# Kernel optimization log

Measured on AMD Instinct MI355X. Metric: run time of the kernel, lower is better.

Reference implementation:

```python
import jax, jax.numpy as jnp
import numpy as np

N, S, R, CM = 1, 128, 256, 256
C, CZ = 32, 128


def setup_inputs() -> dict:
    key = jax.random.key(0)
    k1, k2, k3, k4 = jax.random.split(key, 4)
    return {
        "msa_repr": jax.random.normal(k1, (N, S, R, CM), dtype=jnp.float32),
        "left_proj": jax.random.normal(k2, (CM, C), dtype=jnp.float32) * 0.05,
        "right_proj": jax.random.normal(k3, (CM, C), dtype=jnp.float32) * 0.05,
        "out_proj": jax.random.normal(k4, (C * C, CZ), dtype=jnp.float32) * 0.05,
    }


def reference(msa_repr, left_proj, right_proj, out_proj):
    # msa_repr: [N, S, R, CM]
    # Project to left/right activations and move R before S
    # (equivalent to torch matmul + transpose(-2, -3)).
    a = jnp.einsum("nsrm,mc->nrsc", msa_repr, left_proj)   # [N, R, S, C]
    b = jnp.einsum("nsrm,mc->nrsc", msa_repr, right_proj)  # [N, R, S, C]
    # Outer product contracted over the MSA dim S:
    # outer[n, r, t, c, e] = sum_s a[n, r, s, c] * b[n, t, s, e]
    outer = jnp.einsum("nrsc,ntse->nrtce", a, b)            # [N, R, R, C, C]
    n, r, t = outer.shape[:3]
    outer = outer.reshape(n, r, t, C * C)                   # [N, R, R, C*C]
    # Output projection to pair channels cz
    return outer @ out_proj                                 # [N, R, R, CZ]
```

## Files before the change

kernel.cpp:

```cpp
#include <hip/hip_runtime.h>

typedef __bf16 bf16x8 __attribute__((ext_vector_type(8)));
typedef __bf16 bf16x4 __attribute__((ext_vector_type(4)));
typedef float f32x16 __attribute__((ext_vector_type(16)));
typedef float f32x4 __attribute__((ext_vector_type(4)));

constexpr int S = 128, R = 256, CM = 256, C = 32, CZ = 128;

#define MFMA __builtin_amdgcn_mfma_f32_32x32x16_bf16

__device__ __forceinline__ bf16x4 cvt4(float a, float b, float c, float d) {
    bf16x4 r;
    r[0] = (__bf16)a; r[1] = (__bf16)b; r[2] = (__bf16)c; r[3] = (__bf16)d;
    return r;
}

__global__ __launch_bounds__(256) void k_wlr(const float* __restrict__ Lp,
                                             const float* __restrict__ Rp,
                                             __bf16* __restrict__ WLRT) {
    int c = blockIdx.x;
    int m = threadIdx.x;
    const float* src = (c < 32) ? Lp : Rp;
    WLRT[(size_t)c * 256 + m] = (__bf16)src[(size_t)m * 32 + (c & 31)];
}

__global__ __launch_bounds__(256) void k_projw(const float* __restrict__ msa,
                                               const __bf16* __restrict__ WLRT,
                                               const float* __restrict__ W,
                                               __bf16* __restrict__ aTf,
                                               __bf16* __restrict__ bTf,
                                               __bf16* __restrict__ WTf) {
    const int b = blockIdx.x;
    if (b >= 1024) {
        int g = (b - 1024) * 256 + threadIdx.x;
        int cz = g & 127;
        int k = g >> 7;
        int e = k >> 5, c = k & 31;
        float v = W[(size_t)(c * 32 + e) * 128 + cz];
        WTf[((size_t)(k >> 3) * 128 + cz) * 8 + (k & 7)] = (__bf16)v;
        return;
    }

    __shared__ __align__(16) __bf16 As[32 * 256];
    __shared__ __align__(16) char Pp[2 * 4096];
    const int r = b >> 2;
    const int sq = b & 3;
    const int t = threadIdx.x;

#pragma unroll
    for (int it = 0; it < 8; ++it) {
        int idx = it * 256 + t;
        int row = idx >> 6;
        int cg = idx & 63;
        float4 v = *(const float4*)&msa[((size_t)(sq * 32 + row) * R + r) * CM + cg * 4];
        bf16x4 h = cvt4(v.x, v.y, v.z, v.w);
        int P = (cg >> 1) ^ (row & 15);
        *(bf16x4*)((char*)As + row * 512 + P * 16 + (cg & 1) * 8) = h;
    }
    __syncthreads();

    const int w = t >> 6;
    const int l = t & 63;
    const int l31 = t & 31;
    const int kh = (t >> 5) & 1;
    const int sd = w & 1;
    const int ksh = w >> 1;

    f32x16 acc;
#pragma unroll
    for (int q = 0; q < 16; ++q) acc[q] = 0.f;

    const bf16x8* wb = (const bf16x8*)&WLRT[(size_t)(sd * 32 + l31) * 256 + 8 * kh];
    const char* arow = (const char*)As + l31 * 512;

    __builtin_amdgcn_s_setprio(1);
#pragma unroll
    for (int j = 0; j < 8; ++j) {
        int ks = ksh * 8 + j;
        int P = (2 * ks + kh) ^ (l31 & 15);
        bf16x8 af = *(const bf16x8*)(arow + P * 16);
        acc = MFMA(af, wb[2 * ks], acc, 0, 0, 0);
    }
    __builtin_amdgcn_s_setprio(0);

    char* pbase = Pp + (size_t)sd * 4096;
    if (ksh == 1) {
#pragma unroll
        for (int pc = 0; pc < 4; ++pc) {
            f32x4 v;
            v[0] = acc[4 * pc + 0]; v[1] = acc[4 * pc + 1];
            v[2] = acc[4 * pc + 2]; v[3] = acc[4 * pc + 3];
            *(f32x4*)(pbase + ((pc * 64) + l) * 16) = v;
        }
    }
    __syncthreads();
    if (ksh == 0) {
#pragma unroll
        for (int pc = 0; pc < 4; ++pc) {
            f32x4 v = *(const f32x4*)(pbase + ((pc * 64) + l) * 16);
            acc[4 * pc + 0] += v[0]; acc[4 * pc + 1] += v[1];
            acc[4 * pc + 2] += v[2]; acc[4 * pc + 3] += v[3];
        }
        __bf16* dst = sd ? bTf : aTf;
#pragma unroll
        for (int q = 0; q < 4; ++q) {
            size_t base = (size_t)r * 4096 + (size_t)(2 * sq + (q >> 1)) * 512 +
                          (size_t)(q & 1) * 256 + (size_t)l31 * 8 + 4 * kh;
            *(bf16x4*)&dst[base] = cvt4(acc[4 * q + 0], acc[4 * q + 1],
                                        acc[4 * q + 2], acc[4 * q + 3]);
        }
    }
}

__global__ __launch_bounds__(512, 2) void k_main(const __bf16* __restrict__ aTf,
                                                 const __bf16* __restrict__ bTf,
                                                 const __bf16* __restrict__ WTf,
                                                 float* __restrict__ out) {
    __shared__ __align__(16) __bf16 Gs[64 * 1024];

    const int t = threadIdx.x;
    const int w = t >> 6;
    const int l = t & 63;
    const int lane = l & 31;
    const int kh = l >> 5;
    const int r0 = blockIdx.x * 8;
    const int t0 = blockIdx.y * 8;

    const int rg = w & 3;
    const int tg = w >> 2;

    f32x16 acc[2][4];
#pragma unroll
    for (int i = 0; i < 2; ++i)
#pragma unroll
        for (int j = 0; j < 4; ++j)
#pragma unroll
            for (int q = 0; q < 16; ++q) acc[i][j][q] = 0.f;

    const bf16x8* ap0 = (const bf16x8*)aTf + ((size_t)(r0 + 2 * rg + 0) * 512 + kh * 32 + lane);
    const bf16x8* ap1 = (const bf16x8*)aTf + ((size_t)(r0 + 2 * rg + 1) * 512 + kh * 32 + lane);
    const bf16x8* bp0 = (const bf16x8*)bTf + ((size_t)(t0 + 4 * tg + 0) * 512 + kh * 32 + lane);
    const bf16x8* bp1 = (const bf16x8*)bTf + ((size_t)(t0 + 4 * tg + 1) * 512 + kh * 32 + lane);
    const bf16x8* bp2 = (const bf16x8*)bTf + ((size_t)(t0 + 4 * tg + 2) * 512 + kh * 32 + lane);
    const bf16x8* bp3 = (const bf16x8*)bTf + ((size_t)(t0 + 4 * tg + 3) * 512 + kh * 32 + lane);

    bf16x8 Ap[3][2], Bp[3][4];
#pragma unroll
    for (int s = 0; s < 3; ++s) {
        Ap[s][0] = ap0[s * 64]; Ap[s][1] = ap1[s * 64];
        Bp[s][0] = bp0[s * 64]; Bp[s][1] = bp1[s * 64];
        Bp[s][2] = bp2[s * 64]; Bp[s][3] = bp3[s * 64];
    }
#pragma unroll
    for (int ks = 0; ks < 8; ++ks) {
        const int s = ks % 3;
        __builtin_amdgcn_s_setprio(1);
        acc[0][0] = MFMA(Ap[s][0], Bp[s][0], acc[0][0], 0, 0, 0);
        acc[0][1] = MFMA(Ap[s][0], Bp[s][1], acc[0][1], 0, 0, 0);
        acc[0][2] = MFMA(Ap[s][0], Bp[s][2], acc[0][2], 0, 0, 0);
        acc[0][3] = MFMA(Ap[s][0], Bp[s][3], acc[0][3], 0, 0, 0);
        acc[1][0] = MFMA(Ap[s][1], Bp[s][0], acc[1][0], 0, 0, 0);
        acc[1][1] = MFMA(Ap[s][1], Bp[s][1], acc[1][1], 0, 0, 0);
        acc[1][2] = MFMA(Ap[s][1], Bp[s][2], acc[1][2], 0, 0, 0);
        acc[1][3] = MFMA(Ap[s][1], Bp[s][3], acc[1][3], 0, 0, 0);
        __builtin_amdgcn_s_setprio(0);
        if (ks + 3 < 8) {
            const int kn = ks + 3;
            Ap[s][0] = ap0[kn * 64]; Ap[s][1] = ap1[kn * 64];
            Bp[s][0] = bp0[kn * 64]; Bp[s][1] = bp1[kn * 64];
            Bp[s][2] = bp2[kn * 64]; Bp[s][3] = bp3[kn * 64];
        }
    }

    const int kq = w >> 1;
    const int ng = w & 1;
    const int czl0 = ng * 64 + lane;
    const int czl1 = czl0 + 32;
    const char* wb0c = (const char*)WTf + ((size_t)kh * 128 + czl0) * 16;
    const char* wb1c = (const char*)WTf + ((size_t)kh * 128 + czl1) * 16;

    bf16x8 Wp[16][2];
#pragma unroll
    for (int i = 0; i < 2; ++i) {
#pragma unroll
        for (int j = 0; j < 4; ++j) {
            int p = (2 * rg + i) * 8 + 4 * tg + j;
            unsigned prow = (unsigned)p * 2048;
#pragma unroll
            for (int q = 0; q < 4; ++q) {
                int Lc = lane * 4 + q;
                int P = Lc ^ (p & 15) ^ (lane & 7);
                *(bf16x4*)((char*)Gs + prow + (unsigned)P * 16 + kh * 8) =
                    cvt4(acc[i][j][4 * q + 0], acc[i][j][4 * q + 1],
                         acc[i][j][4 * q + 2], acc[i][j][4 * q + 3]);
            }
            {
                const int u = i * 4 + j;
                const char* a0 = wb0c + (size_t)(kq * 16 + 2 * u) * 4096;
                const char* a1 = wb1c + (size_t)(kq * 16 + 2 * u) * 4096;
                const char* a2 = wb0c + (size_t)(kq * 16 + 2 * u + 1) * 4096;
                const char* a3 = wb1c + (size_t)(kq * 16 + 2 * u + 1) * 4096;
                asm volatile("global_load_dwordx4 %0, %1, off" : "=v"(Wp[2 * u][0]) : "v"(a0));
                asm volatile("global_load_dwordx4 %0, %1, off" : "=v"(Wp[2 * u][1]) : "v"(a1));
                asm volatile("global_load_dwordx4 %0, %1, off" : "=v"(Wp[2 * u + 1][0]) : "v"(a2));
                asm volatile("global_load_dwordx4 %0, %1, off" : "=v"(Wp[2 * u + 1][1]) : "v"(a3));
            }
        }
    }

    asm volatile("s_waitcnt lgkmcnt(0)" ::: "memory");
    __builtin_amdgcn_s_barrier();
    __builtin_amdgcn_sched_barrier(0);

    const unsigned prow0 = (unsigned)lane * 2048;
    const unsigned prow1 = (unsigned)(lane + 32) * 2048;
    const int p15 = lane & 15;

    f32x16 o00, o01, o10, o11;
#pragma unroll
    for (int q = 0; q < 16; ++q) { o00[q] = 0.f; o01[q] = 0.f; o10[q] = 0.f; o11[q] = 0.f; }

    bf16x8 Gp[4][2];
#define LDG(sl, kk) do { \
    int Lr = (kk) * 2 + kh; \
    int P = Lr ^ p15 ^ ((Lr >> 2) & 7); \
    Gp[sl][0] = *(const bf16x8*)((const char*)Gs + prow0 + (unsigned)P * 16); \
    Gp[sl][1] = *(const bf16x8*)((const char*)Gs + prow1 + (unsigned)P * 16); } while (0)

    LDG(0, kq * 16 + 0);
    LDG(1, kq * 16 + 1);
    LDG(2, kq * 16 + 2);
    LDG(3, kq * 16 + 3);

#define STEPB(j, cnt) do { \
    asm volatile("s_waitcnt vmcnt(" #cnt ")"); \
    __builtin_amdgcn_sched_barrier(0); \
    __builtin_amdgcn_s_setprio(1); \
    o00 = MFMA(Gp[(j) & 3][0], Wp[j][0], o00, 0, 0, 0); \
    o01 = MFMA(Gp[(j) & 3][0], Wp[j][1], o01, 0, 0, 0); \
    o10 = MFMA(Gp[(j) & 3][1], Wp[j][0], o10, 0, 0, 0); \
    o11 = MFMA(Gp[(j) & 3][1], Wp[j][1], o11, 0, 0, 0); \
    __builtin_amdgcn_s_setprio(0); \
    if ((j) + 4 < 16) LDG((j) & 3, kq * 16 + (j) + 4); \
} while (0)

    STEPB(0, 30);  STEPB(1, 28);  STEPB(2, 26);  STEPB(3, 24);
    STEPB(4, 22);  STEPB(5, 20);  STEPB(6, 18);  STEPB(7, 16);
    STEPB(8, 14);  STEPB(9, 12);  STEPB(10, 10); STEPB(11, 8);
    STEPB(12, 6);  STEPB(13, 4);  STEPB(14, 2);  STEPB(15, 0);

    __syncthreads();

    {
        char* pr = (char*)Gs + (size_t)w * 16384;
        const f32x16* os[4] = {&o00, &o01, &o10, &o11};
#pragma unroll
        for (int s2 = 0; s2 < 4; ++s2) {
#pragma unroll
            for (int pc = 0; pc < 4; ++pc) {
                f32x4 v;
                v[0] = (*os[s2])[4 * pc + 0]; v[1] = (*os[s2])[4 * pc + 1];
                v[2] = (*os[s2])[4 * pc + 2]; v[3] = (*os[s2])[4 * pc + 3];
                *(f32x4*)(pr + ((s2 * 4 + pc) * 64 + l) * 16) = v;
            }
        }
    }
    __syncthreads();

    {
        const int ngx = w >> 2;
        const int mix = (w >> 1) & 1;
        const int nix = w & 1;
        const int s2 = mix * 2 + nix;
        f32x16 sm;
#pragma unroll
        for (int q = 0; q < 16; ++q) sm[q] = 0.f;
#pragma unroll
        for (int kq2 = 0; kq2 < 4; ++kq2) {
            const char* pr = (const char*)Gs + (size_t)(kq2 * 2 + ngx) * 16384;
#pragma unroll
            for (int pc = 0; pc < 4; ++pc) {
                f32x4 v = *(const f32x4*)(pr + ((s2 * 4 + pc) * 64 + l) * 16);
                sm[4 * pc + 0] += v[0]; sm[4 * pc + 1] += v[1];
                sm[4 * pc + 2] += v[2]; sm[4 * pc + 3] += v[3];
            }
        }
        const int czl = ngx * 64 + nix * 32 + (l & 31);
        const int khx = l >> 5;
#pragma unroll
        for (int reg = 0; reg < 16; ++reg) {
            int pl = mix * 32 + (reg & 3) + 8 * (reg >> 2) + 4 * khx;
            int prr = pl >> 3, ptt = pl & 7;
            out[((size_t)(r0 + prr) * 256 + (t0 + ptt)) * 128 + czl] = sm[reg];
        }
    }
}

extern "C" void kernel_launch(void* const* d_in, const int* in_sizes, int n_in,
                              void* d_out, int out_size, void* d_ws, size_t ws_size,
                              hipStream_t stream) {
    const float* msa = (const float*)d_in[0];
    const float* left = (const float*)d_in[1];
    const float* right = (const float*)d_in[2];
    const float* W = (const float*)d_in[3];

    __bf16* aTf = (__bf16*)d_ws;
    __bf16* bTf = aTf + (size_t)R * 4096;
    __bf16* WTf = bTf + (size_t)R * 4096;
    __bf16* WLRT = WTf + (size_t)128 * 1024;
    float* outp = (float*)d_out;

    k_wlr<<<64, 256, 0, stream>>>(left, right, WLRT);
    k_projw<<<1536, 256, 0, stream>>>(msa, WLRT, W, aTf, bTf, WTf);
    k_main<<<dim3(32, 32), 512, 0, stream>>>(aTf, bTf, WTf, outp);
}
```

Baseline: 59.32 us.

## Repartition output-projection K split across waves to shrink cross-wave reduction

The second GEMM (outer-product tile times out_proj) now splits the K dimension two ways instead of four, with each wave owning one 32-wide cz slice. W fragments are streamed through an 8-deep rolling register buffer instead of being preloaded as 32 registers. This removes one of the shared-memory partial-sum round trips and replaces a four-way reduction with a two-way one, so less LDS traffic and fewer registers are needed. In exchange each wave runs a longer serial MFMA chain and depends more on W load latency being hidden.

Measured after the change: 58.12 us (median of 2 runs). 1.02x faster.

```diff
diff --git a/kernel.cpp b/kernel.cpp
--- a/kernel.cpp
+++ b/kernel.cpp
@@ -172,14 +172,12 @@
         }
     }
 
-    const int kq = w >> 1;
-    const int ng = w & 1;
-    const int czl0 = ng * 64 + lane;
-    const int czl1 = czl0 + 32;
-    const char* wb0c = (const char*)WTf + ((size_t)kh * 128 + czl0) * 16;
-    const char* wb1c = (const char*)WTf + ((size_t)kh * 128 + czl1) * 16;
-
-    bf16x8 Wp[16][2];
+    const int kq = w >> 2;
+    const int ng = w & 3;
+    const int czl = ng * 32 + lane;
+    const char* wbc = (const char*)WTf + ((size_t)kh * 128 + czl) * 16;
+
+    bf16x8 Wp[8];
 #pragma unroll
     for (int i = 0; i < 2; ++i) {
 #pragma unroll
@@ -196,14 +194,8 @@
             }
             {
                 const int u = i * 4 + j;
-                const char* a0 = wb0c + (size_t)(kq * 16 + 2 * u) * 4096;
-                const char* a1 = wb1c + (size_t)(kq * 16 + 2 * u) * 4096;
-                const char* a2 = wb0c + (size_t)(kq * 16 + 2 * u + 1) * 4096;
-                const char* a3 = wb1c + (size_t)(kq * 16 + 2 * u + 1) * 4096;
-                asm volatile("global_load_dwordx4 %0, %1, off" : "=v"(Wp[2 * u][0]) : "v"(a0));
-                asm volatile("global_load_dwordx4 %0, %1, off" : "=v"(Wp[2 * u][1]) : "v"(a1));
-                asm volatile("global_load_dwordx4 %0, %1, off" : "=v"(Wp[2 * u + 1][0]) : "v"(a2));
-                asm volatile("global_load_dwordx4 %0, %1, off" : "=v"(Wp[2 * u + 1][1]) : "v"(a3));
+                asm volatile("global_load_dwordx4 %0, %1, off"
+                             : "=v"(Wp[u]) : "v"(wbc + (size_t)(kq * 32 + u) * 4096));
             }
         }
     }
@@ -216,82 +208,81 @@
     const unsigned prow1 = (unsigned)(lane + 32) * 2048;
     const int p15 = lane & 15;
 
-    f32x16 o00, o01, o10, o11;
-#pragma unroll
-    for (int q = 0; q < 16; ++q) { o00[q] = 0.f; o01[q] = 0.f; o10[q] = 0.f; o11[q] = 0.f; }
+    f32x16 o0, o1;
+#pragma unroll
+    for (int q = 0; q < 16; ++q) { o0[q] = 0.f; o1[q] = 0.f; }
 
     bf16x8 Gp[4][2];
-#define LDG(sl, kk) do { \
-    int Lr = (kk) * 2 + kh; \
+#define LDG(sl, j) do { \
+    int Lr = (kq * 32 + (j)) * 2 + kh; \
     int P = Lr ^ p15 ^ ((Lr >> 2) & 7); \
     Gp[sl][0] = *(const bf16x8*)((const char*)Gs + prow0 + (unsigned)P * 16); \
     Gp[sl][1] = *(const bf16x8*)((const char*)Gs + prow1 + (unsigned)P * 16); } while (0)
 
-    LDG(0, kq * 16 + 0);
-    LDG(1, kq * 16 + 1);
-    LDG(2, kq * 16 + 2);
-    LDG(3, kq * 16 + 3);
+    LDG(0, 0); LDG(1, 1); LDG(2, 2); LDG(3, 3);
 
 #define STEPB(j, cnt) do { \
     asm volatile("s_waitcnt vmcnt(" #cnt ")"); \
     __builtin_amdgcn_sched_barrier(0); \
     __builtin_amdgcn_s_setprio(1); \
-    o00 = MFMA(Gp[(j) & 3][0], Wp[j][0], o00, 0, 0, 0); \
-    o01 = MFMA(Gp[(j) & 3][0], Wp[j][1], o01, 0, 0, 0); \
-    o10 = MFMA(Gp[(j) & 3][1], Wp[j][0], o10, 0, 0, 0); \
-    o11 = MFMA(Gp[(j) & 3][1], Wp[j][1], o11, 0, 0, 0); \
+    o0 = MFMA(Gp[(j) & 3][0], Wp[(j) & 7], o0, 0, 0, 0); \
+    o1 = MFMA(Gp[(j) & 3][1], Wp[(j) & 7], o1, 0, 0, 0); \
     __builtin_amdgcn_s_setprio(0); \
-    if ((j) + 4 < 16) LDG((j) & 3, kq * 16 + (j) + 4); \
+    if ((j) + 8 < 32) { \
+        asm volatile("global_load_dwordx4 %0, %1, off" \
+                     : "=v"(Wp[(j) & 7]) \
+                     : "v"(wbc + (size_t)(kq * 32 + (j) + 8) * 4096)); \
+    } \
+    if ((j) + 4 < 32) LDG((j) & 3, (j) + 4); \
 } while (0)
 
-    STEPB(0, 30);  STEPB(1, 28);  STEPB(2, 26);  STEPB(3, 24);
-    STEPB(4, 22);  STEPB(5, 20);  STEPB(6, 18);  STEPB(7, 16);
-    STEPB(8, 14);  STEPB(9, 12);  STEPB(10, 10); STEPB(11, 8);
-    STEPB(12, 6);  STEPB(13, 4);  STEPB(14, 2);  STEPB(15, 0);
-
-    __syncthreads();
-
-    {
-        char* pr = (char*)Gs + (size_t)w * 16384;
-        const f32x16* os[4] = {&o00, &o01, &o10, &o11};
-#pragma unroll
-        for (int s2 = 0; s2 < 4; ++s2) {
-#pragma unroll
-            for (int pc = 0; pc < 4; ++pc) {
-                f32x4 v;
-                v[0] = (*os[s2])[4 * pc + 0]; v[1] = (*os[s2])[4 * pc + 1];
-                v[2] = (*os[s2])[4 * pc + 2]; v[3] = (*os[s2])[4 * pc + 3];
-                *(f32x4*)(pr + ((s2 * 4 + pc) * 64 + l) * 16) = v;
-            }
-        }
-    }
-    __syncthreads();
-
-    {
-        const int ngx = w >> 2;
-        const int mix = (w >> 1) & 1;
-        const int nix = w & 1;
-        const int s2 = mix * 2 + nix;
-        f32x16 sm;
-#pragma unroll
-        for (int q = 0; q < 16; ++q) sm[q] = 0.f;
-#pragma unroll
-        for (int kq2 = 0; kq2 < 4; ++kq2) {
-            const char* pr = (const char*)Gs + (size_t)(kq2 * 2 + ngx) * 16384;
-#pragma unroll
-            for (int pc = 0; pc < 4; ++pc) {
-                f32x4 v = *(const f32x4*)(pr + ((s2 * 4 + pc) * 64 + l) * 16);
-                sm[4 * pc + 0] += v[0]; sm[4 * pc + 1] += v[1];
-                sm[4 * pc + 2] += v[2]; sm[4 * pc + 3] += v[3];
-            }
-        }
-        const int czl = ngx * 64 + nix * 32 + (l & 31);
-        const int khx = l >> 5;
+    STEPB(0, 7);  STEPB(1, 7);  STEPB(2, 7);  STEPB(3, 7);
+    STEPB(4, 7);  STEPB(5, 7);  STEPB(6, 7);  STEPB(7, 7);
+    STEPB(8, 7);  STEPB(9, 7);  STEPB(10, 7); STEPB(11, 7);
+    STEPB(12, 7); STEPB(13, 7); STEPB(14, 7); STEPB(15, 7);
+    STEPB(16, 7); STEPB(17, 7); STEPB(18, 7); STEPB(19, 7);
+    STEPB(20, 7); STEPB(21, 7); STEPB(22, 7); STEPB(23, 7);
+    STEPB(24, 7); STEPB(25, 6); STEPB(26, 5); STEPB(27, 4);
+    STEPB(28, 3); STEPB(29, 2); STEPB(30, 1); STEPB(31, 0);
+
+    asm volatile("s_waitcnt lgkmcnt(0)");
+    __builtin_amdgcn_s_barrier();
+
+    if (kq == 1) {
+        char* p0 = (char*)Gs + (size_t)(ng * 2 + 0) * 4096;
+        char* p1 = (char*)Gs + (size_t)(ng * 2 + 1) * 4096;
+#pragma unroll
+        for (int pc = 0; pc < 4; ++pc) {
+            f32x4 v0, v1;
+            v0[0] = o0[4 * pc + 0]; v0[1] = o0[4 * pc + 1];
+            v0[2] = o0[4 * pc + 2]; v0[3] = o0[4 * pc + 3];
+            v1[0] = o1[4 * pc + 0]; v1[1] = o1[4 * pc + 1];
+            v1[2] = o1[4 * pc + 2]; v1[3] = o1[4 * pc + 3];
+            *(f32x4*)(p0 + (pc * 64 + l) * 16) = v0;
+            *(f32x4*)(p1 + (pc * 64 + l) * 16) = v1;
+        }
+    }
+    asm volatile("s_waitcnt lgkmcnt(0)");
+    __builtin_amdgcn_s_barrier();
+
+    if (kq == 0) {
+        const char* p0 = (const char*)Gs + (size_t)(ng * 2 + 0) * 4096;
+        const char* p1 = (const char*)Gs + (size_t)(ng * 2 + 1) * 4096;
+#pragma unroll
+        for (int pc = 0; pc < 4; ++pc) {
+            f32x4 v0 = *(const f32x4*)(p0 + (pc * 64 + l) * 16);
+            f32x4 v1 = *(const f32x4*)(p1 + (pc * 64 + l) * 16);
+            o0[4 * pc + 0] += v0[0]; o0[4 * pc + 1] += v0[1];
+            o0[4 * pc + 2] += v0[2]; o0[4 * pc + 3] += v0[3];
+            o1[4 * pc + 0] += v1[0]; o1[4 * pc + 1] += v1[1];
+            o1[4 * pc + 2] += v1[2]; o1[4 * pc + 3] += v1[3];
+        }
 #pragma unroll
         for (int reg = 0; reg < 16; ++reg) {
-            int pl = mix * 32 + (reg & 3) + 8 * (reg >> 2) + 4 * khx;
-            int prr = pl >> 3, ptt = pl & 7;
-            out[((size_t)(r0 + prr) * 256 + (t0 + ptt)) * 128 + czl] = sm[reg];
+            int pl = (reg & 3) + 8 * (reg >> 2) + 4 * kh;
+            int p0r = pl, p1r = 32 + pl;
+            out[((size_t)(r0 + (p0r >> 3)) * 256 + (t0 + (p0r & 7))) * 128 + czl] = o0[reg];
+            out[((size_t)(r0 + (p1r >> 3)) * 256 + (t0 + (p1r & 7))) * 128 + czl] = o1[reg];
         }
     }
 }
```
